# Kernel optimization log

Hardware: AMD Instinct MI355X
Metric: run time of the kernel (lower is better)

The kernel has to match this reference:

```python
import jax, jax.numpy as jnp
import numpy as np

D = 512
H = 8
DH = D // H


def setup_inputs() -> dict:
    key = jax.random.key(0)
    ks = jax.random.split(key, 6)
    B, S = 2, 4096
    scale = 1.0 / np.sqrt(D)
    x = jax.random.normal(ks[0], (B, S, D), dtype=jnp.float32)
    W_q = jax.random.normal(ks[1], (D, D), dtype=jnp.float32) * scale
    W_k = jax.random.normal(ks[2], (D, D), dtype=jnp.float32) * scale
    W_v = jax.random.normal(ks[3], (D, D), dtype=jnp.float32) * scale
    W_proj = jax.random.normal(ks[4], (D, D), dtype=jnp.float32) * scale
    b_proj = jax.random.normal(ks[5], (D,), dtype=jnp.float32) * 0.01
    return {"x": x, "W_q": W_q, "W_k": W_k, "W_v": W_v,
            "W_proj": W_proj, "b_proj": b_proj}


def reference(x, W_q, W_k, W_v, W_proj, b_proj):
    B, S, _ = x.shape
    # torch Linear: y = x @ W.T
    def proj(W):
        y = jnp.einsum('bsd,ed->bse', x, W)
        return y.reshape(B, S, H, DH).transpose(0, 2, 1, 3)  # [B,H,S,DH]
    q, k, v = proj(W_q), proj(W_k), proj(W_v)
    scores = jnp.einsum('bhqd,bhkd->bhqk', q, k) / np.sqrt(DH)  # [B,H,S,S]
    causal = jnp.tril(jnp.ones((S, S), dtype=bool))
    neg = jnp.finfo(scores.dtype).min
    scores = jnp.where(causal[None, None, :, :], scores, neg)
    w = jax.nn.softmax(scores, axis=-1)
    attn = jnp.einsum('bhqk,bhkd->bhqd', w, v)  # [B,H,S,DH]
    attn = attn.transpose(0, 2, 1, 3).reshape(B, S, D)
    return jnp.einsum('bsd,ed->bse', attn, W_proj) + b_proj
```

## Files before the change

kernel.cpp:

```cpp
#include <hip/hip_runtime.h>
#include <hip/hip_bf16.h>
#include <stdint.h>

#define D_MODEL 512
#define NH 8
#define DH 64
#define SEQ 4096
#define NBH 16

typedef __attribute__((ext_vector_type(8))) short bf16x8;
typedef __attribute__((ext_vector_type(4))) float f32x4;
typedef __attribute__((ext_vector_type(16))) float f32x16;

#define CSCALE 0.18033688011112042f

__device__ __forceinline__ uint32_t pkbf(float a, float b) {
    uint32_t r;
    asm("v_cvt_pk_bf16_f32 %0, %1, %2" : "=v"(r) : "v"(a), "v"(b));
    return r;
}

#define SWZ(R) (((R) + ((R) >> 2)) & 3)

#define BAR() do {                                          \
    asm volatile("s_waitcnt lgkmcnt(0)" ::: "memory");      \
    __builtin_amdgcn_s_barrier();                           \
} while (0)

__device__ __forceinline__ bf16x8 cvt8(float4 u, float4 v, float s) {
    union { uint32_t w[4]; bf16x8 h; } r;
    r.w[0] = pkbf(u.x * s, u.y * s); r.w[1] = pkbf(u.z * s, u.w * s);
    r.w[2] = pkbf(v.x * s, v.y * s); r.w[3] = pkbf(v.z * s, v.w * s);
    return r.h;
}

__global__ __launch_bounds__(256) void qkv_kernel(
    const float* __restrict__ x,
    const float* __restrict__ Wq, const float* __restrict__ Wk,
    const float* __restrict__ Wv,
    short* __restrict__ Qb, short* __restrict__ Kb, short* __restrict__ Vt)
{
    __shared__ __align__(16) short at[2][4096];
    __shared__ __align__(16) short bt[2][4096];

    const int tid  = threadIdx.x;
    const int wave = tid >> 6;
    const int lane = tid & 63;
    const int ln = lane & 15, quad = lane >> 4;
    const int z = blockIdx.z;
    const float* W = (z == 0) ? Wq : (z == 1) ? Wk : Wv;
    const float wscale = (z == 0) ? CSCALE : 1.0f;
    const int m0 = blockIdx.x * 128;
    const int n0 = blockIdx.y * 128;
    const int mh = (wave & 1) * 64, nh = (wave >> 1) * 64;

    const int ck0 = tid, ck1 = tid + 256;
    const int R0 = ck0 >> 2, R1 = ck1 >> 2;
    const int c0 = (ck0 & 3) ^ SWZ(R0), c1 = (ck1 & 3) ^ SWZ(R1);

    float4 ra[4], rb[4];
    auto loadAB = [&](int kc) {
        const float* pa0 = x + (size_t)(m0 + R0) * D_MODEL + kc + c0 * 8;
        const float* pa1 = x + (size_t)(m0 + R1) * D_MODEL + kc + c1 * 8;
        ra[0] = *(const float4*)pa0; ra[1] = *(const float4*)(pa0 + 4);
        ra[2] = *(const float4*)pa1; ra[3] = *(const float4*)(pa1 + 4);
        const float* pb0 = W + (size_t)(n0 + R0) * D_MODEL + kc + c0 * 8;
        const float* pb1 = W + (size_t)(n0 + R1) * D_MODEL + kc + c1 * 8;
        rb[0] = *(const float4*)pb0; rb[1] = *(const float4*)(pb0 + 4);
        rb[2] = *(const float4*)pb1; rb[3] = *(const float4*)(pb1 + 4);
    };
    auto writeAB = [&](int buf) {
        *(bf16x8*)&at[buf][ck0 * 8] = cvt8(ra[0], ra[1], 1.0f);
        *(bf16x8*)&at[buf][ck1 * 8] = cvt8(ra[2], ra[3], 1.0f);
        *(bf16x8*)&bt[buf][ck0 * 8] = cvt8(rb[0], rb[1], wscale);
        *(bf16x8*)&bt[buf][ck1 * 8] = cvt8(rb[2], rb[3], wscale);
    };

    f32x4 acc[4][4] = {};

    loadAB(0);
    writeAB(0);

    for (int s = 0; s < 16; ++s) {
        const int cur = s & 1;
        BAR();
        if (s < 15) loadAB((s + 1) * 32);

        bf16x8 a[4], b[4];
#pragma unroll
        for (int i = 0; i < 4; ++i) {
            const int R = mh + i * 16 + ln;
            a[i] = *(const bf16x8*)(&at[cur][R * 32 + ((quad ^ SWZ(R)) * 8)]);
        }
#pragma unroll
        for (int j = 0; j < 4; ++j) {
            const int R = nh + j * 16 + ln;
            b[j] = *(const bf16x8*)(&bt[cur][R * 32 + ((quad ^ SWZ(R)) * 8)]);
        }
#pragma unroll
        for (int i = 0; i < 4; ++i)
#pragma unroll
            for (int j = 0; j < 4; ++j)
                acc[i][j] = __builtin_amdgcn_mfma_f32_16x16x32_bf16(
                    a[i], b[j], acc[i][j], 0, 0, 0);

        if (s < 15) writeAB(cur ^ 1);
    }

    if (z == 2) {
#pragma unroll
        for (int i = 0; i < 4; ++i) {
            const int row0 = m0 + mh + i * 16 + quad * 4;
            const int bb = row0 >> 12, sq = row0 & (SEQ - 1);
#pragma unroll
            for (int j = 0; j < 4; ++j) {
                const int n = n0 + nh + j * 16 + ln;
                const int h = n >> 6, dh = n & 63;
                uint2 st;
                st.x = pkbf(acc[i][j][0], acc[i][j][1]);
                st.y = pkbf(acc[i][j][2], acc[i][j][3]);
                *(uint2*)(Vt + (size_t)((bb * NH + h) * DH + dh) * SEQ + sq) = st;
            }
        }
    } else {
        short* P = (z == 0) ? Qb : Kb;
#pragma unroll
        for (int i = 0; i < 4; ++i)
#pragma unroll
            for (int j = 0; j < 4; ++j) {
                const int n = n0 + nh + j * 16 + ln;
                const int h = n >> 6, dh = n & 63;
                const uint32_t lo = pkbf(acc[i][j][0], acc[i][j][1]);
                const uint32_t hi2 = pkbf(acc[i][j][2], acc[i][j][3]);
#pragma unroll
                for (int r = 0; r < 4; ++r) {
                    const int row = m0 + mh + i * 16 + quad * 4 + r;
                    const int bb = row >> 12, sq = row & (SEQ - 1);
                    const uint32_t w = (r < 2) ? lo : hi2;
                    P[((size_t)((bb * NH + h) * SEQ + sq) << 6) + dh] =
                        (short)((r & 1) ? (w >> 16) : (w & 0xffff));
                }
            }
    }
}

__global__ __launch_bounds__(256) void attn_kernel(
    const short* __restrict__ Qb, const short* __restrict__ Kb,
    const short* __restrict__ Vt, short* __restrict__ ao)
{
    __shared__ __align__(16) short kt[2][4096];
    __shared__ __align__(16) short vt[2][4096];

    const int tid  = threadIdx.x;
    const int wave = tid >> 6;
    const int lane = tid & 63;
    const int l31 = lane & 31, hi = lane >> 5;
    const int bh = blockIdx.y;
    const int w_ = (blockIdx.x + 4 * bh) & 31;
    const int g2 = ((bh >> 3) & 1) ? (31 - w_) : w_;
    const short* Qp = Qb + (size_t)bh * SEQ * DH;
    const short* Kp = Kb + (size_t)bh * SEQ * DH;
    const short* Vp = Vt + (size_t)bh * DH * SEQ;
    const int bb = bh >> 3, h = bh & 7;
    const int q0 = g2 * 128 + wave * 32;
    const int myq = q0 + l31;
    const int jdiag = q0 >> 6;
    const int jmax = 2 * g2 + 1;

    const int ckA = tid, ckB = tid + 256;
    const int RA = ckA >> 3, RB = ckB >> 3;
    const int cA = (ckA & 7) ^ (RA & 7), cB = (ckB & 7) ^ (RB & 7);
    const int RA31 = RA & 31, RB31 = RB & 31;
    const int kkA = (RA & 32) + ((RA31 & 8) << 1) + ((RA31 & 4) << 1)
                  + ((RA31 & 16) >> 2) + (RA31 & 3);
    const int kkB = (RB & 32) + ((RB31 & 8) << 1) + ((RB31 & 4) << 1)
                  + ((RB31 & 16) >> 2) + (RB31 & 3);
    const size_t kOffA = ((size_t)kkA << 6) + cA * 8;
    const size_t kOffB = ((size_t)kkB << 6) + cB * 8;
    const size_t vOffA = (size_t)RA * SEQ + cA * 8;
    const size_t vOffB = (size_t)RB * SEQ + cB * 8;

    bf16x8 sk0, sk1, sv0, sv1;
    auto load_tile = [&](int j) {
        const size_t k0 = (size_t)j * 64;
        sk0 = *(const bf16x8*)(Kp + (k0 << 6) + kOffA);
        sk1 = *(const bf16x8*)(Kp + (k0 << 6) + kOffB);
        sv0 = *(const bf16x8*)(Vp + vOffA + k0);
        sv1 = *(const bf16x8*)(Vp + vOffB + k0);
    };
    auto write_tile = [&](int buf) {
        *(bf16x8*)&kt[buf][ckA * 8] = sk0;
        *(bf16x8*)&kt[buf][ckB * 8] = sk1;
        *(bf16x8*)&vt[buf][ckA * 8] = sv0;
        *(bf16x8*)&vt[buf][ckB * 8] = sv1;
    };

    bf16x8 qf[4];
#pragma unroll
    for (int c = 0; c < 4; ++c)
        qf[c] = *(const bf16x8*)(Qp + (size_t)myq * DH + c * 16 + hi * 8);

    const bf16x8 ones = { (short)0x3F80, (short)0x3F80, (short)0x3F80,
                          (short)0x3F80, (short)0x3F80, (short)0x3F80,
                          (short)0x3F80, (short)0x3F80 };

    f32x16 o0 = {}, o1 = {};
    f32x16 lacc = {};

    load_tile(0);
    write_tile(0);
    load_tile(1);
    BAR();

    for (int j = 0; j <= jmax; ++j) {
        const int cur = j & 1;
        if (j < jmax) {
            write_tile(cur ^ 1);
            if (j + 1 < jmax) load_tile(j + 2);
        }

        if ((j << 6) <= q0 + 31) {
            f32x16 s0 = {}, s1 = {};
            const int sw = l31 & 7;
            __builtin_amdgcn_s_setprio(1);
#pragma unroll
            for (int c = 0; c < 4; ++c) {
                const int pc = ((2 * c + hi) ^ sw) * 8;
                bf16x8 a0 = *(const bf16x8*)(&kt[cur][l31 * 64 + pc]);
                bf16x8 a1 = *(const bf16x8*)(&kt[cur][(32 + l31) * 64 + pc]);
                s0 = __builtin_amdgcn_mfma_f32_32x32x16_bf16(a0, qf[c], s0, 0, 0, 0);
                s1 = __builtin_amdgcn_mfma_f32_32x32x16_bf16(a1, qf[c], s1, 0, 0, 0);
            }
            __builtin_amdgcn_s_setprio(0);
            if (j >= jdiag) {
                const int k0 = j * 64;
#pragma unroll
                for (int reg = 0; reg < 16; ++reg) {
                    const int kl = ((reg >> 2) & 1) * 16 + hi * 8
                                 + ((reg >> 3) & 1) * 4 + (reg & 3);
                    if (k0 + kl > myq)      s0[reg] = -3e38f;
                    if (k0 + 32 + kl > myq) s1[reg] = -3e38f;
                }
            }
#pragma unroll
            for (int i = 0; i < 16; ++i) {
                s0[i] = __builtin_amdgcn_exp2f(s0[i]);
                s1[i] = __builtin_amdgcn_exp2f(s1[i]);
            }

            union { uint32_t u[4]; bf16x8 v; } p00, p01, p10, p11;
            p00.u[0] = pkbf(s0[0], s0[1]);   p00.u[1] = pkbf(s0[2], s0[3]);
            p00.u[2] = pkbf(s0[8], s0[9]);   p00.u[3] = pkbf(s0[10], s0[11]);
            p01.u[0] = pkbf(s0[4], s0[5]);   p01.u[1] = pkbf(s0[6], s0[7]);
            p01.u[2] = pkbf(s0[12], s0[13]); p01.u[3] = pkbf(s0[14], s0[15]);
            p10.u[0] = pkbf(s1[0], s1[1]);   p10.u[1] = pkbf(s1[2], s1[3]);
            p10.u[2] = pkbf(s1[8], s1[9]);   p10.u[3] = pkbf(s1[10], s1[11]);
            p11.u[0] = pkbf(s1[4], s1[5]);   p11.u[1] = pkbf(s1[6], s1[7]);
            p11.u[2] = pkbf(s1[12], s1[13]); p11.u[3] = pkbf(s1[14], s1[15]);

            __builtin_amdgcn_s_setprio(1);
            lacc = __builtin_amdgcn_mfma_f32_32x32x16_bf16(ones, p00.v, lacc, 0, 0, 0);
            lacc = __builtin_amdgcn_mfma_f32_32x32x16_bf16(ones, p01.v, lacc, 0, 0, 0);
            lacc = __builtin_amdgcn_mfma_f32_32x32x16_bf16(ones, p10.v, lacc, 0, 0, 0);
            lacc = __builtin_amdgcn_mfma_f32_32x32x16_bf16(ones, p11.v, lacc, 0, 0, 0);

            {
                const short* vrow = &vt[cur][l31 * 64];
                bf16x8 v00 = *(const bf16x8*)(vrow + (((0 + hi) ^ sw) * 8));
                bf16x8 v01 = *(const bf16x8*)(vrow + (((2 + hi) ^ sw) * 8));
                bf16x8 v10 = *(const bf16x8*)(vrow + (((4 + hi) ^ sw) * 8));
                bf16x8 v11 = *(const bf16x8*)(vrow + (((6 + hi) ^ sw) * 8));
                o0 = __builtin_amdgcn_mfma_f32_32x32x16_bf16(v00, p00.v, o0, 0, 0, 0);
                o0 = __builtin_amdgcn_mfma_f32_32x32x16_bf16(v01, p01.v, o0, 0, 0, 0);
                o0 = __builtin_amdgcn_mfma_f32_32x32x16_bf16(v10, p10.v, o0, 0, 0, 0);
                o0 = __builtin_amdgcn_mfma_f32_32x32x16_bf16(v11, p11.v, o0, 0, 0, 0);
            }
            {
                const short* vrow = &vt[cur][(32 + l31) * 64];
                bf16x8 v00 = *(const bf16x8*)(vrow + (((0 + hi) ^ sw) * 8));
                bf16x8 v01 = *(const bf16x8*)(vrow + (((2 + hi) ^ sw) * 8));
                bf16x8 v10 = *(const bf16x8*)(vrow + (((4 + hi) ^ sw) * 8));
                bf16x8 v11 = *(const bf16x8*)(vrow + (((6 + hi) ^ sw) * 8));
                o1 = __builtin_amdgcn_mfma_f32_32x32x16_bf16(v00, p00.v, o1, 0, 0, 0);
                o1 = __builtin_amdgcn_mfma_f32_32x32x16_bf16(v01, p01.v, o1, 0, 0, 0);
                o1 = __builtin_amdgcn_mfma_f32_32x32x16_bf16(v10, p10.v, o1, 0, 0, 0);
                o1 = __builtin_amdgcn_mfma_f32_32x32x16_bf16(v11, p11.v, o1, 0, 0, 0);
            }
            __builtin_amdgcn_s_setprio(0);
        }
        BAR();
    }
    const float inv = 1.0f / lacc[0];
    short* orow = ao + (size_t)(bb * SEQ + myq) * D_MODEL + h * DH;
#pragma unroll
    for (int c = 0; c < 4; ++c) {
        uint2 st;
        st.x = pkbf(o0[4 * c] * inv,     o0[4 * c + 1] * inv);
        st.y = pkbf(o0[4 * c + 2] * inv, o0[4 * c + 3] * inv);
        *(uint2*)(orow + 8 * c + 4 * hi) = st;
    }
#pragma unroll
    for (int c = 0; c < 4; ++c) {
        uint2 st;
        st.x = pkbf(o1[4 * c] * inv,     o1[4 * c + 1] * inv);
        st.y = pkbf(o1[4 * c + 2] * inv, o1[4 * c + 3] * inv);
        *(uint2*)(orow + 32 + 8 * c + 4 * hi) = st;
    }
}

__global__ __launch_bounds__(256) void proj_kernel(
    const short* __restrict__ attn, const float* __restrict__ Wp,
    const float* __restrict__ bias, float* __restrict__ out)
{
    __shared__ __align__(16) short at[2][2048];
    __shared__ __align__(16) short bt[2][4096];

    const int tid  = threadIdx.x;
    const int wave = tid >> 6;
    const int lane = tid & 63;
    const int ln = lane & 15, quad = lane >> 4;
    const int m0 = blockIdx.x * 64;
    const int n0 = blockIdx.y * 128;
    const int mh = (wave & 1) * 32, nh = (wave >> 1) * 64;

    const int RA = tid >> 2, cAc = (tid & 3) ^ SWZ(RA);
    const int ck0 = tid, ck1 = tid + 256;
    const int R0 = ck0 >> 2, R1 = ck1 >> 2;
    const int c0 = (ck0 & 3) ^ SWZ(R0), c1 = (ck1 & 3) ^ SWZ(R1);

    bf16x8 raA;
    float4 rb[4];
    auto loadAB = [&](int kc) {
        raA = *(const bf16x8*)(attn + (size_t)(m0 + RA) * D_MODEL + kc + cAc * 8);
        const float* pb0 = Wp + (size_t)(n0 + R0) * D_MODEL + kc + c0 * 8;
        const float* pb1 = Wp + (size_t)(n0 + R1) * D_MODEL + kc + c1 * 8;
        rb[0] = *(const float4*)pb0; rb[1] = *(const float4*)(pb0 + 4);
        rb[2] = *(const float4*)pb1; rb[3] = *(const float4*)(pb1 + 4);
    };
    auto writeAB = [&](int buf) {
        *(bf16x8*)&at[buf][tid * 8] = raA;
        *(bf16x8*)&bt[buf][ck0 * 8] = cvt8(rb[0], rb[1], 1.0f);
        *(bf16x8*)&bt[buf][ck1 * 8] = cvt8(rb[2], rb[3], 1.0f);
    };

    f32x4 acc[2][4] = {};

    loadAB(0);
    writeAB(0);

    for (int s = 0; s < 16; ++s) {
        const int cur = s & 1;
        BAR();
        if (s < 15) loadAB((s + 1) * 32);

        bf16x8 a[2], b[4];
#pragma unroll
        for (int i = 0; i < 2; ++i) {
            const int R = mh + i * 16 + ln;
            a[i] = *(const bf16x8*)(&at[cur][R * 32 + ((quad ^ SWZ(R)) * 8)]);
        }
#pragma unroll
        for (int j = 0; j < 4; ++j) {
            const int R = nh + j * 16 + ln;
            b[j] = *(const bf16x8*)(&bt[cur][R * 32 + ((quad ^ SWZ(R)) * 8)]);
        }
#pragma unroll
        for (int i = 0; i < 2; ++i)
#pragma unroll
            for (int j = 0; j < 4; ++j)
                acc[i][j] = __builtin_amdgcn_mfma_f32_16x16x32_bf16(
                    a[i], b[j], acc[i][j], 0, 0, 0);

        if (s < 15) writeAB(cur ^ 1);
    }
#pragma unroll
    for (int j = 0; j < 4; ++j) {
        const int n = n0 + nh + j * 16 + ln;
        const float bv = bias[n];
#pragma unroll
        for (int i = 0; i < 2; ++i)
#pragma unroll
            for (int r = 0; r < 4; ++r) {
                const int row = m0 + mh + i * 16 + quad * 4 + r;
                out[(size_t)row * D_MODEL + n] = acc[i][j][r] + bv;
            }
    }
}

extern "C" void kernel_launch(void* const* d_in, const int* in_sizes, int n_in,
                              void* d_out, int out_size, void* d_ws, size_t ws_size,
                              hipStream_t stream) {
    const float* x  = (const float*)d_in[0];
    const float* Wq = (const float*)d_in[1];
    const float* Wk = (const float*)d_in[2];
    const float* Wv = (const float*)d_in[3];
    const float* Wp = (const float*)d_in[4];
    const float* bp = (const float*)d_in[5];
    float* out = (float*)d_out;

    short* Qb = (short*)d_ws;
    short* Kb = Qb + (size_t)NBH * SEQ * DH;
    short* Vt = Kb + (size_t)NBH * SEQ * DH;
    short* ab = Vt + (size_t)NBH * SEQ * DH;

    qkv_kernel<<<dim3(64, 4, 3), 256, 0, stream>>>(x, Wq, Wk, Wv, Qb, Kb, Vt);
    attn_kernel<<<dim3(32, NBH), 256, 0, stream>>>(Qb, Kb, Vt, ab);
    proj_kernel<<<dim3(128, 4), 256, 0, stream>>>(ab, Wp, bp, out);
}
```

Measured before the change: 171.2 us.

## Pre-convert inputs and weights to bf16 in a separate pass, add MFMA priority

Adds a conversion kernel that turns x and all four weight matrices into bf16 once, with the softmax scale folded into W_q. The converted x is staged in the output buffer and the weights in the workspace. The QKV and projection GEMMs then load bf16 directly, halving their global read bytes and dropping the per-tile fp32-to-bf16 conversion, which matters because qkv re-reads x once per output column tile. It also raises wave priority around the MFMA blocks. The cost is an extra launch and an extra full pass over x.

Result: no change. 169.4 us (-1.1%).

```diff
diff --git a/kernel.cpp b/kernel.cpp
--- a/kernel.cpp
+++ b/kernel.cpp
@@ -7,6 +7,8 @@
 #define DH 64
 #define SEQ 4096
 #define NBH 16
+#define NX  (2 * SEQ * D_MODEL)
+#define NW  (D_MODEL * D_MODEL)
 
 typedef __attribute__((ext_vector_type(8))) short bf16x8;
 typedef __attribute__((ext_vector_type(4))) float f32x4;
@@ -34,10 +36,31 @@
     return r.h;
 }
 
-__global__ __launch_bounds__(256) void qkv_kernel(
+__global__ __launch_bounds__(256) void cvt_pre(
     const float* __restrict__ x,
     const float* __restrict__ Wq, const float* __restrict__ Wk,
-    const float* __restrict__ Wv,
+    const float* __restrict__ Wv, const float* __restrict__ Wp,
+    short* __restrict__ xb, short* __restrict__ Wb)
+{
+    const size_t t = ((size_t)blockIdx.x * 256 + threadIdx.x) * 8;
+    const float* src; short* dst; float s = 1.0f; size_t off;
+    if (t < NX) {
+        src = x; dst = xb; off = t;
+    } else {
+        const size_t u = t - NX;
+        const int w = (int)(u >> 18);
+        off = u & (NW - 1);
+        src = (w == 0) ? Wq : (w == 1) ? Wk : (w == 2) ? Wv : Wp;
+        dst = Wb + ((size_t)w << 18);
+        s = (w == 0) ? CSCALE : 1.0f;
+    }
+    float4 a = *(const float4*)(src + off);
+    float4 b = *(const float4*)(src + off + 4);
+    *(bf16x8*)(dst + off) = cvt8(a, b, s);
+}
+
+__global__ __launch_bounds__(256) void qkv_kernel(
+    const short* __restrict__ xb, const short* __restrict__ Wb,
     short* __restrict__ Qb, short* __restrict__ Kb, short* __restrict__ Vt)
 {
     __shared__ __align__(16) short at[2][4096];
@@ -48,8 +71,7 @@
     const int lane = tid & 63;
     const int ln = lane & 15, quad = lane >> 4;
     const int z = blockIdx.z;
-    const float* W = (z == 0) ? Wq : (z == 1) ? Wk : Wv;
-    const float wscale = (z == 0) ? CSCALE : 1.0f;
+    const short* W = Wb + ((size_t)z << 18);
     const int m0 = blockIdx.x * 128;
     const int n0 = blockIdx.y * 128;
     const int mh = (wave & 1) * 64, nh = (wave >> 1) * 64;
@@ -58,22 +80,18 @@
     const int R0 = ck0 >> 2, R1 = ck1 >> 2;
     const int c0 = (ck0 & 3) ^ SWZ(R0), c1 = (ck1 & 3) ^ SWZ(R1);
 
-    float4 ra[4], rb[4];
+    bf16x8 ra0, ra1, rb0, rb1;
     auto loadAB = [&](int kc) {
-        const float* pa0 = x + (size_t)(m0 + R0) * D_MODEL + kc + c0 * 8;
-        const float* pa1 = x + (size_t)(m0 + R1) * D_MODEL + kc + c1 * 8;
-        ra[0] = *(const float4*)pa0; ra[1] = *(const float4*)(pa0 + 4);
-        ra[2] = *(const float4*)pa1; ra[3] = *(const float4*)(pa1 + 4);
-        const float* pb0 = W + (size_t)(n0 + R0) * D_MODEL + kc + c0 * 8;
-        const float* pb1 = W + (size_t)(n0 + R1) * D_MODEL + kc + c1 * 8;
-        rb[0] = *(const float4*)pb0; rb[1] = *(const float4*)(pb0 + 4);
-        rb[2] = *(const float4*)pb1; rb[3] = *(const float4*)(pb1 + 4);
+        ra0 = *(const bf16x8*)(xb + (size_t)(m0 + R0) * D_MODEL + kc + c0 * 8);
+        ra1 = *(const bf16x8*)(xb + (size_t)(m0 + R1) * D_MODEL + kc + c1 * 8);
+        rb0 = *(const bf16x8*)(W + (size_t)(n0 + R0) * D_MODEL + kc + c0 * 8);
+        rb1 = *(const bf16x8*)(W + (size_t)(n0 + R1) * D_MODEL + kc + c1 * 8);
     };
     auto writeAB = [&](int buf) {
-        *(bf16x8*)&at[buf][ck0 * 8] = cvt8(ra[0], ra[1], 1.0f);
-        *(bf16x8*)&at[buf][ck1 * 8] = cvt8(ra[2], ra[3], 1.0f);
-        *(bf16x8*)&bt[buf][ck0 * 8] = cvt8(rb[0], rb[1], wscale);
-        *(bf16x8*)&bt[buf][ck1 * 8] = cvt8(rb[2], rb[3], wscale);
+        *(bf16x8*)&at[buf][ck0 * 8] = ra0;
+        *(bf16x8*)&at[buf][ck1 * 8] = ra1;
+        *(bf16x8*)&bt[buf][ck0 * 8] = rb0;
+        *(bf16x8*)&bt[buf][ck1 * 8] = rb1;
     };
 
     f32x4 acc[4][4] = {};
@@ -97,12 +115,14 @@
             const int R = nh + j * 16 + ln;
             b[j] = *(const bf16x8*)(&bt[cur][R * 32 + ((quad ^ SWZ(R)) * 8)]);
         }
+        __builtin_amdgcn_s_setprio(1);
 #pragma unroll
         for (int i = 0; i < 4; ++i)
 #pragma unroll
             for (int j = 0; j < 4; ++j)
                 acc[i][j] = __builtin_amdgcn_mfma_f32_16x16x32_bf16(
                     a[i], b[j], acc[i][j], 0, 0, 0);
+        __builtin_amdgcn_s_setprio(0);
 
         if (s < 15) writeAB(cur ^ 1);
     }
@@ -309,7 +329,7 @@
 }
 
 __global__ __launch_bounds__(256) void proj_kernel(
-    const short* __restrict__ attn, const float* __restrict__ Wp,
+    const short* __restrict__ attn, const short* __restrict__ Wpb,
     const float* __restrict__ bias, float* __restrict__ out)
 {
     __shared__ __align__(16) short at[2][2048];
@@ -328,19 +348,16 @@
     const int R0 = ck0 >> 2, R1 = ck1 >> 2;
     const int c0 = (ck0 & 3) ^ SWZ(R0), c1 = (ck1 & 3) ^ SWZ(R1);
 
-    bf16x8 raA;
-    float4 rb[4];
+    bf16x8 raA, rb0, rb1;
     auto loadAB = [&](int kc) {
         raA = *(const bf16x8*)(attn + (size_t)(m0 + RA) * D_MODEL + kc + cAc * 8);
-        const float* pb0 = Wp + (size_t)(n0 + R0) * D_MODEL + kc + c0 * 8;
-        const float* pb1 = Wp + (size_t)(n0 + R1) * D_MODEL + kc + c1 * 8;
-        rb[0] = *(const float4*)pb0; rb[1] = *(const float4*)(pb0 + 4);
-        rb[2] = *(const float4*)pb1; rb[3] = *(const float4*)(pb1 + 4);
+        rb0 = *(const bf16x8*)(Wpb + (size_t)(n0 + R0) * D_MODEL + kc + c0 * 8);
+        rb1 = *(const bf16x8*)(Wpb + (size_t)(n0 + R1) * D_MODEL + kc + c1 * 8);
     };
     auto writeAB = [&](int buf) {
         *(bf16x8*)&at[buf][tid * 8] = raA;
-        *(bf16x8*)&bt[buf][ck0 * 8] = cvt8(rb[0], rb[1], 1.0f);
-        *(bf16x8*)&bt[buf][ck1 * 8] = cvt8(rb[2], rb[3], 1.0f);
+        *(bf16x8*)&bt[buf][ck0 * 8] = rb0;
+        *(bf16x8*)&bt[buf][ck1 * 8] = rb1;
     };
 
     f32x4 acc[2][4] = {};
@@ -364,12 +381,14 @@
             const int R = nh + j * 16 + ln;
             b[j] = *(const bf16x8*)(&bt[cur][R * 32 + ((quad ^ SWZ(R)) * 8)]);
         }
+        __builtin_amdgcn_s_setprio(1);
 #pragma unroll
         for (int i = 0; i < 2; ++i)
 #pragma unroll
             for (int j = 0; j < 4; ++j)
                 acc[i][j] = __builtin_amdgcn_mfma_f32_16x16x32_bf16(
                     a[i], b[j], acc[i][j], 0, 0, 0);
+        __builtin_amdgcn_s_setprio(0);
 
         if (s < 15) writeAB(cur ^ 1);
     }
@@ -402,8 +421,13 @@
     short* Kb = Qb + (size_t)NBH * SEQ * DH;
     short* Vt = Kb + (size_t)NBH * SEQ * DH;
     short* ab = Vt + (size_t)NBH * SEQ * DH;
-
-    qkv_kernel<<<dim3(64, 4, 3), 256, 0, stream>>>(x, Wq, Wk, Wv, Qb, Kb, Vt);
+    short* Wb = ab + (size_t)NBH * SEQ * DH;
+
+    short* xb = (short*)d_out;
+
+    cvt_pre<<<dim3((NX + 4 * NW) / (8 * 256)), 256, 0, stream>>>(
+        x, Wq, Wk, Wv, Wp, xb, Wb);
+    qkv_kernel<<<dim3(64, 4, 3), 256, 0, stream>>>(xb, Wb, Qb, Kb, Vt);
     attn_kernel<<<dim3(32, NBH), 256, 0, stream>>>(Qb, Kb, Vt, ab);
-    proj_kernel<<<dim3(128, 4), 256, 0, stream>>>(ab, Wp, bp, out);
-}
+    proj_kernel<<<dim3(128, 4), 256, 0, stream>>>(ab, Wb + 3 * (size_t)NW, bp, out);
+}
```
